# Kernel optimization log

Hardware: AMD Instinct MI355X
Metric: run time of the kernel (lower is better)

The kernel has to match this reference:

```python
import jax, jax.numpy as jnp
import numpy as np

T, B, E, H = 2048, 2, 1024, 16
D = E // H

def setup_inputs() -> dict:
    key = jax.random.key(0)
    ks = jax.random.split(key, 5)
    s = 1.0 / np.sqrt(E)  # keep projection weights at sane scale
    return {
        "query": jax.random.normal(ks[0], (T, B, E), jnp.float32),
        "Wq": jax.random.normal(ks[1], (E, E), jnp.float32) * s,
        "bq": jnp.zeros((E,), jnp.float32),
        "Wk": jax.random.normal(ks[2], (E, E), jnp.float32) * s,
        "bk": jnp.zeros((E,), jnp.float32),
        "Wv": jax.random.normal(ks[3], (E, E), jnp.float32) * s,
        "bv": jnp.zeros((E,), jnp.float32),
        "Wo": jax.random.normal(ks[4], (E, E), jnp.float32) * s,
        "bo": jnp.zeros((E,), jnp.float32),
    }

def reference(query, Wq, bq, Wk, bk, Wv, bv, Wo, bo):
    # query: [T, B, E] (fairseq time-first). self-attention path.
    scaling = D ** -0.5
    q = (query @ Wq.T + bq) * scaling          # [T,B,E]
    k = query @ Wk.T + bk                      # [T,B,E]
    v = query @ Wv.T + bv                      # [T,B,E]
    # split heads: [T,B,H,D]
    q = q.reshape(T, B, H, D)
    k = k.reshape(T, B, H, D)
    v = v.reshape(T, B, H, D)
    # attention scores [B,H,T,S]
    scores = jnp.einsum("tbhd,sbhd->bhts", q, k)
    probs = jax.nn.softmax(scores, axis=-1)
    # weighted values -> [T,B,H,D]
    attn = jnp.einsum("bhts,sbhd->tbhd", probs, v).reshape(T, B, E)
    return attn @ Wo.T + bo                    # [T,B,E]
```

## Files before the change

### kernel.cpp

```cpp
#include <hip/hip_runtime.h>
#include <hip/hip_bf16.h>

#define T_DIM 2048

typedef __attribute__((ext_vector_type(8))) short short8_t;
typedef short8_t __attribute__((may_alias)) short8_a;
typedef __attribute__((ext_vector_type(4))) short short4_t;
typedef short4_t __attribute__((may_alias)) short4_a;
typedef __attribute__((ext_vector_type(4))) float f32x4;
typedef __attribute__((ext_vector_type(16))) float f32x16;
typedef __attribute__((ext_vector_type(4))) float float4_t;
typedef float4_t __attribute__((may_alias)) float4_a;
typedef __attribute__((ext_vector_type(4))) unsigned int u32x4;

__device__ __forceinline__ short f2bf(float f) {
    unsigned int u = __builtin_bit_cast(unsigned int, f);
    unsigned int r = (u + 0x7fffu + ((u >> 16) & 1u)) >> 16;
    return (short)r;
}

__device__ __forceinline__ void gl_lds16(const short* g, short* l) {
    __builtin_amdgcn_global_load_lds(
        (const __attribute__((address_space(1))) void*)g,
        (__attribute__((address_space(3))) void*)l, 16, 0, 0);
}

__global__ __launch_bounds__(256) void cvt_all(const float* __restrict__ query,
                                               const float* __restrict__ Wq,
                                               const float* __restrict__ Wk,
                                               const float* __restrict__ Wv,
                                               const float* __restrict__ Wo,
                                               short* __restrict__ out) {
    const int bx = blockIdx.x;
    const int i = bx * 2048 + threadIdx.x * 8;
    const float* s;
    if (bx < 2048) {
        s = query + i;
    } else {
        int j = i - 4194304;
        int wsel = j >> 20;
        const float* wp = wsel == 0 ? Wq : (wsel == 1 ? Wk : (wsel == 2 ? Wv : Wo));
        s = wp + (j & 1048575);
    }
    float4_a a = *(const float4_a*)s;
    float4_a b = *(const float4_a*)(s + 4);
    short8_a r;
    r[0] = f2bf(a[0]); r[1] = f2bf(a[1]); r[2] = f2bf(a[2]); r[3] = f2bf(a[3]);
    r[4] = f2bf(b[0]); r[5] = f2bf(b[1]); r[6] = f2bf(b[2]); r[7] = f2bf(b[3]);
    *(short8_a*)(out + i) = r;
}

template <int BM, int BN, int MODE>
__global__ __launch_bounds__(256) void gemm_lds(const short* __restrict__ A,
                                                const short* __restrict__ W,
                                                const float* __restrict__ b0,
                                                const float* __restrict__ b1,
                                                const float* __restrict__ b2,
                                                short* __restrict__ o0,
                                                short* __restrict__ o1,
                                                short* __restrict__ o2,
                                                float* __restrict__ of) {
    constexpr int FM = BM / 32;
    constexpr int FN = BN / 32;
    __shared__ short As[BM * 32];
    __shared__ short Bs[BN * 32];

    const int tid = threadIdx.x;
    const int l = tid & 63, w = tid >> 6;
    const int wm = w >> 1, wn = w & 1;
    const int m0 = blockIdx.y * BM, n0 = blockIdx.x * BN;
    const int l15 = l & 15, l4 = l >> 4;
    const int lr = l >> 2, lc = (l & 3) * 8;

    f32x4 acc[FM][FN];
#pragma unroll
    for (int i = 0; i < FM; i++)
#pragma unroll
        for (int j = 0; j < FN; j++) {
            f32x4 z = {0.f, 0.f, 0.f, 0.f};
            acc[i][j] = z;
        }

    const short* Ab = A + (m0 + lr) * 1024 + lc;
    const short* Wb = W + (n0 + lr) * 1024 + lc;

    for (int k0 = 0; k0 < 1024; k0 += 32) {
#pragma unroll
        for (int j = 0; j < BM / 64; j++) {
            int base = (j * 4 + w) * 16;
            gl_lds16(Ab + base * 1024 + k0, &As[base * 32]);
        }
#pragma unroll
        for (int j = 0; j < BN / 64; j++) {
            int base = (j * 4 + w) * 16;
            gl_lds16(Wb + base * 1024 + k0, &Bs[base * 32]);
        }
        __syncthreads();

        short8_t af[FM], bf[FN];
#pragma unroll
        for (int m = 0; m < FM; m++)
            af[m] = *(const short8_a*)&As[(wm * (BM / 2) + m * 16 + l15) * 32 + l4 * 8];
#pragma unroll
        for (int n = 0; n < FN; n++)
            bf[n] = *(const short8_a*)&Bs[(wn * (BN / 2) + n * 16 + l15) * 32 + l4 * 8];
#pragma unroll
        for (int m = 0; m < FM; m++)
#pragma unroll
            for (int n = 0; n < FN; n++)
                acc[m][n] = __builtin_amdgcn_mfma_f32_16x16x32_bf16(af[m], bf[n], acc[m][n], 0, 0, 0);
        __syncthreads();
    }

    if (MODE == 3) {
#pragma unroll
        for (int n = 0; n < FN; n++) {
            int col = n0 + wn * (BN / 2) + n * 16 + l15;
            float bv = b0[col];
#pragma unroll
            for (int m = 0; m < FM; m++)
#pragma unroll
                for (int i = 0; i < 4; i++) {
                    int row = m0 + wm * (BM / 2) + m * 16 + l4 * 4 + i;
                    of[row * 1024 + col] = acc[m][n][i] + bv;
                }
        }
    } else {
        const int proj = n0 >> 10;
        const float* bias = proj == 0 ? b0 : (proj == 1 ? b1 : b2);
        short* outp = proj == 0 ? o0 : (proj == 1 ? o1 : o2);
#pragma unroll
        for (int n = 0; n < FN; n++) {
            int cw = (n0 + wn * (BN / 2) + n * 16 + l15) & 1023;
            float bv = bias[cw];
            int h = cw >> 6, d = cw & 63;
#pragma unroll
            for (int m = 0; m < FM; m++)
#pragma unroll
                for (int i = 0; i < 4; i++) {
                    int row = m0 + wm * (BM / 2) + m * 16 + l4 * 4 + i;
                    float v = acc[m][n][i] + bv;
                    if (proj == 0) v *= 0.18033688011112042f;
                    int bb = row & 1, t = row >> 1;
                    if (proj == 2)
                        outp[((bb * 16 + h) * 64 + d) * 2048 + t] = f2bf(v);
                    else
                        outp[((bb * 16 + h) * 2048 + t) * 64 + d] = f2bf(v);
                }
        }
    }
}

__global__ __launch_bounds__(256) void flash_attn(const short* __restrict__ Q,
                                                  const short* __restrict__ K,
                                                  const short* __restrict__ Vt,
                                                  short* __restrict__ O) {
    __shared__ short Ks[4][64 * 64];
    __shared__ short Vs[4][64 * 64];

    const int tid = threadIdx.x, l = tid & 63, w = tid >> 6;
    const int l31 = l & 31, hi = l >> 5;
    const int e = l31 & 7;

    const int bid = blockIdx.x + (blockIdx.y << 4);
    const int swz = (bid & 7) * 64 + (bid >> 3);
    const int qt = swz & 15, bh = swz >> 4;

    const int b = bh >> 4, hh = bh & 15;
    const int qrow = qt * 128 + w * 32 + l31;

    const short* Qp = Q + bh * (T_DIM * 64);
    const short* Kp = K + bh * (T_DIM * 64);
    const short* Vp = Vt + bh * (64 * T_DIM);

    short8_t qf[4];
#pragma unroll
    for (int c = 0; c < 4; c++)
        qf[c] = *(const short8_a*)&Qp[qrow * 64 + c * 16 + hi * 8];

    f32x16 oacc[2];
    f32x16 lacc;
    f32x16 zro;
#pragma unroll
    for (int i = 0; i < 16; i++) { oacc[0][i] = 0.f; oacc[1][i] = 0.f; lacc[i] = 0.f; zro[i] = 0.f; }

    short8_t ones;
#pragma unroll
    for (int j = 0; j < 8; j++) ones[j] = (short)0x3F80;

    const int lrow = l >> 3;
    const int lch = (l & 7) ^ (lrow & 7);
    const int j0 = 2 * w, j1 = 2 * w + 1;
    const short* kg0 = Kp + (j0 * 8 + lrow) * 64 + lch * 8;
    const short* kg1 = Kp + (j1 * 8 + lrow) * 64 + lch * 8;
    const short* vg0 = Vp + (j0 * 8 + lrow) * 2048 + lch * 8;
    const short* vg1 = Vp + (j1 * 8 + lrow) * 2048 + lch * 8;

    auto stage = [&](int it) {
        const int buf = it & 3;
        const int koff = it * 4096, voff = it * 64;
        gl_lds16(kg0 + koff, &Ks[buf][j0 * 512]);
        gl_lds16(kg1 + koff, &Ks[buf][j1 * 512]);
        gl_lds16(vg0 + voff, &Vs[buf][j0 * 512]);
        gl_lds16(vg1 + voff, &Vs[buf][j1 * 512]);
    };

    auto qk = [&](f32x16* st, int t) {
        const short* kc = &Ks[t & 3][0];
#pragma unroll
        for (int c = 0; c < 4; c++) {
            short8_t kf0 = *(const short8_a*)&kc[(l31) * 64 + ((2 * c + hi) ^ e) * 8];
            short8_t kf1 = *(const short8_a*)&kc[(32 + l31) * 64 + ((2 * c + hi) ^ e) * 8];
            st[0] = __builtin_amdgcn_mfma_f32_32x32x16_bf16(kf0, qf[c], c == 0 ? zro : st[0], 0, 0, 0);
            st[1] = __builtin_amdgcn_mfma_f32_32x32x16_bf16(kf1, qf[c], c == 0 ? zro : st[1], 0, 0, 0);
        }
    };

    auto pv = [&](const short8_t* pf, int t) {
        const short* vc = &Vs[t & 3][0];
#pragma unroll
        for (int r = 0; r < 2; r++)
#pragma unroll
            for (int cc = 0; cc < 2; cc++) {
                short8_t p = pf[r * 2 + cc];
                lacc = __builtin_amdgcn_mfma_f32_32x32x16_bf16(ones, p, lacc, 0, 0, 0);
#pragma unroll
                for (int dd = 0; dd < 2; dd++) {
                    short8_t vf = *(const short8_a*)&vc[(dd * 32 + l31) * 64 +
                                                        ((4 * r + 2 * cc + hi) ^ e) * 8];
                    oacc[dd] = __builtin_amdgcn_mfma_f32_32x32x16_bf16(vf, p, oacc[dd], 0, 0, 0);
                }
            }
    };

    auto expack = [&](f32x16* st, short8_t* pf) {
#pragma unroll
        for (int r = 0; r < 2; r++) {
#pragma unroll
            for (int i = 0; i < 16; i++) st[r][i] = exp2f(st[r][i]);
            unsigned pk8[8];
#pragma unroll
            for (int u = 0; u < 8; u++) {
                unsigned t;
                asm("v_cvt_pk_bf16_f32 %0, %1, %2" : "=v"(t) : "v"(st[r][2 * u]), "v"(st[r][2 * u + 1]));
                pk8[u] = t;
            }
#pragma unroll
            for (int cc = 0; cc < 2; cc++) {
                unsigned A0 = pk8[4 * cc + 0], B0 = pk8[4 * cc + 2];
                unsigned A1 = pk8[4 * cc + 1], B1 = pk8[4 * cc + 3];
                asm("v_permlane32_swap_b32 %0, %1" : "+v"(A0), "+v"(B0));
                asm("v_permlane32_swap_b32 %0, %1" : "+v"(A1), "+v"(B1));
                u32x4 pu = {A0, A1, B0, B1};
                pf[r * 2 + cc] = __builtin_bit_cast(short8_t, pu);
            }
        }
    };

    f32x16 stA[2], stB[2];
    short8_t pfA[4], pfB[4];

    stage(0);
    __syncthreads();
    stage(1);
    qk(stB, 0);

    auto halfiter = [&](f32x16* stCur, f32x16* stNext, short8_t* pfIn, short8_t* pfOut, int i) {
        __syncthreads();
        if (i + 2 < 32) stage(i + 2);
        __builtin_amdgcn_s_setprio(1);
        if (i + 1 < 32) qk(stNext, i + 1);
        if (i > 0) pv(pfIn, i - 1);
        __builtin_amdgcn_s_setprio(0);
        expack(stCur, pfOut);
    };

    for (int i = 0; i < 32; i += 2) {
        halfiter(stB, stA, pfA, pfB, i);
        halfiter(stA, stB, pfB, pfA, i + 1);
    }
    pv(pfA, 31);

    float rl = 1.0f / lacc[0];
#pragma unroll
    for (int dd = 0; dd < 2; dd++)
#pragma unroll
        for (int g = 0; g < 4; g++) {
            short4_t o4;
#pragma unroll
            for (int i = 0; i < 4; i++) o4[i] = f2bf(oacc[dd][4 * g + i] * rl);
            *(short4_a*)&O[(qrow * 2 + b) * 1024 + hh * 64 + dd * 32 + g * 8 + hi * 4] = o4;
        }
}

extern "C" void kernel_launch(void* const* d_in, const int* in_sizes, int n_in,
                              void* d_out, int out_size, void* d_ws, size_t ws_size,
                              hipStream_t stream) {
    const float* query = (const float*)d_in[0];
    const float* Wq = (const float*)d_in[1];
    const float* bq = (const float*)d_in[2];
    const float* Wk = (const float*)d_in[3];
    const float* bk = (const float*)d_in[4];
    const float* Wv = (const float*)d_in[5];
    const float* bv = (const float*)d_in[6];
    const float* Wo = (const float*)d_in[7];
    const float* bo = (const float*)d_in[8];

    short* Xbf = (short*)d_ws;
    short* Wqb = Xbf + 4194304;
    short* Wkb = Wqb + 1048576;
    short* Wvb = Wkb + 1048576;
    short* Wob = Wvb + 1048576;
    short* Qb = Wob + 1048576;
    short* Kb = Qb + 4194304;
    short* Vtb = Kb + 4194304;
    short* attnb = Xbf;

    cvt_all<<<4096, 256, 0, stream>>>(query, Wq, Wk, Wv, Wo, Xbf);

    gemm_lds<128, 128, 4><<<dim3(24, 32), 256, 0, stream>>>(Xbf, Wqb, bq, bk, bv,
                                                            Qb, Kb, Vtb, nullptr);

    flash_attn<<<dim3(16, 32), 256, 0, stream>>>(Qb, Kb, Vtb, attnb);

    gemm_lds<64, 128, 3><<<dim3(8, 64), 256, 0, stream>>>(attnb, Wob, bo, nullptr, nullptr,
                                                          nullptr, nullptr, nullptr, (float*)d_out);
}
```

Measured before the change: 133.0 us.

## Process two KV tiles per barrier in flash attention and swizzle GEMM block order

```diff
diff --git a/kernel.cpp b/kernel.cpp
--- a/kernel.cpp
+++ b/kernel.cpp
@@ -68,7 +68,14 @@
     const int tid = threadIdx.x;
     const int l = tid & 63, w = tid >> 6;
     const int wm = w >> 1, wn = w & 1;
-    const int m0 = blockIdx.y * BM, n0 = blockIdx.x * BN;
+
+    const int nbx = gridDim.x;
+    const int nb = nbx * gridDim.y;
+    const int bid = blockIdx.x + nbx * blockIdx.y;
+    const int swz = (bid & 7) * (nb >> 3) + (bid >> 3);
+    const int bx = swz % nbx, by = swz / nbx;
+
+    const int m0 = by * BM, n0 = bx * BN;
     const int l15 = l & 15, l4 = l >> 4;
     const int lr = l >> 2, lc = (l & 3) * 8;
 
@@ -156,7 +163,7 @@
                                                   const short* __restrict__ Vt,
                                                   short* __restrict__ O) {
     __shared__ short Ks[4][64 * 64];
-    __shared__ short Vs[4][64 * 64];
+    __shared__ short Vs[6][64 * 64];
 
     const int tid = threadIdx.x, l = tid & 63, w = tid >> 6;
     const int l31 = l & 31, hi = l >> 5;
@@ -196,13 +203,15 @@
     const short* vg0 = Vp + (j0 * 8 + lrow) * 2048 + lch * 8;
     const short* vg1 = Vp + (j1 * 8 + lrow) * 2048 + lch * 8;
 
-    auto stage = [&](int it) {
-        const int buf = it & 3;
-        const int koff = it * 4096, voff = it * 64;
+    auto stageK = [&](int it) {
+        const int buf = it & 3, koff = it * 4096;
         gl_lds16(kg0 + koff, &Ks[buf][j0 * 512]);
         gl_lds16(kg1 + koff, &Ks[buf][j1 * 512]);
-        gl_lds16(vg0 + voff, &Vs[buf][j0 * 512]);
-        gl_lds16(vg1 + voff, &Vs[buf][j1 * 512]);
+    };
+    auto stageV = [&](int it, int vb) {
+        const int voff = it * 64;
+        gl_lds16(vg0 + voff, &Vs[vb][j0 * 512]);
+        gl_lds16(vg1 + voff, &Vs[vb][j1 * 512]);
     };
 
     auto qk = [&](f32x16* st, int t) {
@@ -216,8 +225,8 @@
         }
     };
 
-    auto pv = [&](const short8_t* pf, int t) {
-        const short* vc = &Vs[t & 3][0];
+    auto pv = [&](const short8_t* pf, int vb) {
+        const short* vc = &Vs[vb][0];
 #pragma unroll
         for (int r = 0; r < 2; r++)
 #pragma unroll
@@ -260,26 +269,35 @@
     f32x16 stA[2], stB[2];
     short8_t pfA[4], pfB[4];
 
-    stage(0);
-    __syncthreads();
-    stage(1);
-    qk(stB, 0);
-
-    auto halfiter = [&](f32x16* stCur, f32x16* stNext, short8_t* pfIn, short8_t* pfOut, int i) {
+    stageK(0); stageV(0, 0);
+    stageK(1); stageV(1, 1);
+
+    int sa = 2, sb = 3, pa = 4, pb = 5;
+
+    for (int p = 0; p < 16; ++p) {
         __syncthreads();
-        if (i + 2 < 32) stage(i + 2);
+        if (p < 15) {
+            stageK(2 * p + 2); stageV(2 * p + 2, sa);
+            stageK(2 * p + 3); stageV(2 * p + 3, sb);
+        }
         __builtin_amdgcn_s_setprio(1);
-        if (i + 1 < 32) qk(stNext, i + 1);
-        if (i > 0) pv(pfIn, i - 1);
+        qk(stA, 2 * p);
+        if (p > 0) pv(pfA, pa);
         __builtin_amdgcn_s_setprio(0);
-        expack(stCur, pfOut);
-    };
-
-    for (int i = 0; i < 32; i += 2) {
-        halfiter(stB, stA, pfA, pfB, i);
-        halfiter(stA, stB, pfB, pfA, i + 1);
+        if (p > 0) expack(stB, pfB);
+        __builtin_amdgcn_s_setprio(1);
+        qk(stB, 2 * p + 1);
+        if (p > 0) pv(pfB, pb);
+        __builtin_amdgcn_s_setprio(0);
+        expack(stA, pfA);
+        sa += 2; if (sa >= 6) sa -= 6;
+        sb += 2; if (sb >= 6) sb -= 6;
+        pa += 2; if (pa >= 6) pa -= 6;
+        pb += 2; if (pb >= 6) pb -= 6;
     }
-    pv(pfA, 31);
+    pv(pfA, pa);
+    expack(stB, pfB);
+    pv(pfB, pb);
 
     float rl = 1.0f / lacc[0];
 #pragma unroll
```

Result: faster. 129.4 us (-2.8%).

## Split attention KV tiles across two wave groups and swizzle GEMM block order

Applied to the files above, without the earlier changes.

```diff
diff --git a/kernel.cpp b/kernel.cpp
--- a/kernel.cpp
+++ b/kernel.cpp
@@ -68,7 +68,14 @@
     const int tid = threadIdx.x;
     const int l = tid & 63, w = tid >> 6;
     const int wm = w >> 1, wn = w & 1;
-    const int m0 = blockIdx.y * BM, n0 = blockIdx.x * BN;
+
+    const int nbx = gridDim.x;
+    const int nb = nbx * gridDim.y;
+    const int bid = blockIdx.x + nbx * blockIdx.y;
+    const int swz = (bid & 7) * (nb >> 3) + (bid >> 3);
+    const int bx = swz % nbx, by = swz / nbx;
+
+    const int m0 = by * BM, n0 = bx * BN;
     const int l15 = l & 15, l4 = l >> 4;
     const int lr = l >> 2, lc = (l & 3) * 8;
 
@@ -151,14 +158,15 @@
     }
 }
 
-__global__ __launch_bounds__(256) void flash_attn(const short* __restrict__ Q,
-                                                  const short* __restrict__ K,
-                                                  const short* __restrict__ Vt,
-                                                  short* __restrict__ O) {
+__global__ __launch_bounds__(512, 4) void flash_attn(const short* __restrict__ Q,
+                                                     const short* __restrict__ K,
+                                                     const short* __restrict__ Vt,
+                                                     short* __restrict__ O) {
     __shared__ short Ks[4][64 * 64];
     __shared__ short Vs[4][64 * 64];
 
     const int tid = threadIdx.x, l = tid & 63, w = tid >> 6;
+    const int w4 = w >> 1, g = w & 1;
     const int l31 = l & 31, hi = l >> 5;
     const int e = l31 & 7;
 
@@ -167,7 +175,7 @@
     const int qt = swz & 15, bh = swz >> 4;
 
     const int b = bh >> 4, hh = bh & 15;
-    const int qrow = qt * 128 + w * 32 + l31;
+    const int qrow = qt * 128 + w4 * 32 + l31;
 
     const short* Qp = Q + bh * (T_DIM * 64);
     const short* Kp = K + bh * (T_DIM * 64);
@@ -180,9 +188,8 @@
 
     f32x16 oacc[2];
     f32x16 lacc;
-    f32x16 zro;
-#pragma unroll
-    for (int i = 0; i < 16; i++) { oacc[0][i] = 0.f; oacc[1][i] = 0.f; lacc[i] = 0.f; zro[i] = 0.f; }
+#pragma unroll
+    for (int i = 0; i < 16; i++) { oacc[0][i] = 0.f; oacc[1][i] = 0.f; lacc[i] = 0.f; }
 
     short8_t ones;
 #pragma unroll
@@ -190,29 +197,43 @@
 
     const int lrow = l >> 3;
     const int lch = (l & 7) ^ (lrow & 7);
-    const int j0 = 2 * w, j1 = 2 * w + 1;
-    const short* kg0 = Kp + (j0 * 8 + lrow) * 64 + lch * 8;
-    const short* kg1 = Kp + (j1 * 8 + lrow) * 64 + lch * 8;
-    const short* vg0 = Vp + (j0 * 8 + lrow) * 2048 + lch * 8;
-    const short* vg1 = Vp + (j1 * 8 + lrow) * 2048 + lch * 8;
-
-    auto stage = [&](int it) {
-        const int buf = it & 3;
-        const int koff = it * 4096, voff = it * 64;
-        gl_lds16(kg0 + koff, &Ks[buf][j0 * 512]);
-        gl_lds16(kg1 + koff, &Ks[buf][j1 * 512]);
-        gl_lds16(vg0 + voff, &Vs[buf][j0 * 512]);
-        gl_lds16(vg1 + voff, &Vs[buf][j1 * 512]);
+    const int wq = w & 3;
+    const int j0 = 2 * wq, j1 = 2 * wq + 1;
+    const short* sg0;
+    const short* sg1;
+    if (w < 4) {
+        sg0 = Kp + (j0 * 8 + lrow) * 64 + lch * 8;
+        sg1 = Kp + (j1 * 8 + lrow) * 64 + lch * 8;
+    } else {
+        sg0 = Vp + (j0 * 8 + lrow) * 2048 + lch * 8;
+        sg1 = Vp + (j1 * 8 + lrow) * 2048 + lch * 8;
+    }
+
+    auto stage = [&](int t) {
+        const int buf = t & 3;
+        if (w < 4) {
+            const int koff = t * 4096;
+            gl_lds16(sg0 + koff, &Ks[buf][j0 * 512]);
+            gl_lds16(sg1 + koff, &Ks[buf][j1 * 512]);
+        } else {
+            const int voff = t * 64;
+            gl_lds16(sg0 + voff, &Vs[buf][j0 * 512]);
+            gl_lds16(sg1 + voff, &Vs[buf][j1 * 512]);
+        }
     };
 
     auto qk = [&](f32x16* st, int t) {
         const short* kc = &Ks[t & 3][0];
+        f32x16 z;
+#pragma unroll
+        for (int i = 0; i < 16; i++) z[i] = 0.f;
+        st[0] = z; st[1] = z;
 #pragma unroll
         for (int c = 0; c < 4; c++) {
             short8_t kf0 = *(const short8_a*)&kc[(l31) * 64 + ((2 * c + hi) ^ e) * 8];
             short8_t kf1 = *(const short8_a*)&kc[(32 + l31) * 64 + ((2 * c + hi) ^ e) * 8];
-            st[0] = __builtin_amdgcn_mfma_f32_32x32x16_bf16(kf0, qf[c], c == 0 ? zro : st[0], 0, 0, 0);
-            st[1] = __builtin_amdgcn_mfma_f32_32x32x16_bf16(kf1, qf[c], c == 0 ? zro : st[1], 0, 0, 0);
+            st[0] = __builtin_amdgcn_mfma_f32_32x32x16_bf16(kf0, qf[c], st[0], 0, 0, 0);
+            st[1] = __builtin_amdgcn_mfma_f32_32x32x16_bf16(kf1, qf[c], st[1], 0, 0, 0);
         }
     };
 
@@ -257,40 +278,54 @@
         }
     };
 
-    f32x16 stA[2], stB[2];
-    short8_t pfA[4], pfB[4];
-
     stage(0);
+    stage(1);
+
+    f32x16 st[2];
+    short8_t pf[4];
+
+    for (int p = 0; p < 16; ++p) {
+        __syncthreads();
+        if (p < 15) { stage(2 * p + 2); stage(2 * p + 3); }
+        const int t = 2 * p + g;
+        __builtin_amdgcn_s_setprio(1);
+        qk(st, t);
+        __builtin_amdgcn_s_setprio(0);
+        expack(st, pf);
+        __builtin_amdgcn_s_setprio(1);
+        pv(pf, t);
+        __builtin_amdgcn_s_setprio(0);
+    }
+
     __syncthreads();
-    stage(1);
-    qk(stB, 0);
-
-    auto halfiter = [&](f32x16* stCur, f32x16* stNext, short8_t* pfIn, short8_t* pfOut, int i) {
-        __syncthreads();
-        if (i + 2 < 32) stage(i + 2);
-        __builtin_amdgcn_s_setprio(1);
-        if (i + 1 < 32) qk(stNext, i + 1);
-        if (i > 0) pv(pfIn, i - 1);
-        __builtin_amdgcn_s_setprio(0);
-        expack(stCur, pfOut);
-    };
-
-    for (int i = 0; i < 32; i += 2) {
-        halfiter(stB, stA, pfA, pfB, i);
-        halfiter(stA, stB, pfB, pfA, i + 1);
-    }
-    pv(pfA, 31);
-
-    float rl = 1.0f / lacc[0];
-#pragma unroll
-    for (int dd = 0; dd < 2; dd++)
-#pragma unroll
-        for (int g = 0; g < 4; g++) {
-            short4_t o4;
-#pragma unroll
-            for (int i = 0; i < 4; i++) o4[i] = f2bf(oacc[dd][4 * g + i] * rl);
-            *(short4_a*)&O[(qrow * 2 + b) * 1024 + hh * 64 + dd * 32 + g * 8 + hi * 4] = o4;
-        }
+    float* xo = (float*)&Ks[0][0];
+    float* xml = (float*)&Vs[0][0];
+    if (g == 1) {
+#pragma unroll
+        for (int dd = 0; dd < 2; dd++)
+#pragma unroll
+            for (int g4 = 0; g4 < 4; g4++) {
+                f32x4 v = {oacc[dd][4 * g4], oacc[dd][4 * g4 + 1],
+                           oacc[dd][4 * g4 + 2], oacc[dd][4 * g4 + 3]};
+                *(float4_a*)&xo[w4 * 2048 + (dd * 4 + g4) * 256 + l * 4] = v;
+            }
+        xml[w4 * 64 + l] = lacc[0];
+    }
+    __syncthreads();
+    if (g == 0) {
+        float rl = 1.0f / (lacc[0] + xml[w4 * 64 + l]);
+#pragma unroll
+        for (int dd = 0; dd < 2; dd++)
+#pragma unroll
+            for (int g4 = 0; g4 < 4; g4++) {
+                f32x4 o1 = *(const float4_a*)&xo[w4 * 2048 + (dd * 4 + g4) * 256 + l * 4];
+                short4_t o4;
+#pragma unroll
+                for (int i = 0; i < 4; i++)
+                    o4[i] = f2bf((oacc[dd][4 * g4 + i] + o1[i]) * rl);
+                *(short4_a*)&O[(qrow * 2 + b) * 1024 + hh * 64 + dd * 32 + g4 * 8 + hi * 4] = o4;
+            }
+    }
 }
 
 extern "C" void kernel_launch(void* const* d_in, const int* in_sizes, int n_in,
@@ -321,7 +356,7 @@
     gemm_lds<128, 128, 4><<<dim3(24, 32), 256, 0, stream>>>(Xbf, Wqb, bq, bk, bv,
                                                             Qb, Kb, Vtb, nullptr);
 
-    flash_attn<<<dim3(16, 32), 256, 0, stream>>>(Qb, Kb, Vtb, attnb);
+    flash_attn<<<dim3(16, 32), 512, 0, stream>>>(Qb, Kb, Vtb, attnb);
 
     gemm_lds<64, 128, 3><<<dim3(8, 64), 256, 0, stream>>>(attnb, Wob, bo, nullptr, nullptr,
                                                           nullptr, nullptr, nullptr, (float*)d_out);
```

Measured after the change: 123.6 us. 7.1% less time.
